# Kernel optimization log

Measured on AMD Instinct MI355X. Metric: run time of the kernel, lower is better.

## Reference

```python
import jax, jax.numpy as jnp
import numpy as np

N, HID, EMB, T_ENC, T_DEC = 10000, 64, 64, 12, 12


def setup_inputs() -> dict:
    key = jax.random.key(0)
    ks = jax.random.split(key, 16)
    s = 0.05  # small init scale (xavier-ish)
    inputs = jax.random.normal(ks[0], (N, T_ENC), dtype=jnp.float32)
    targets = jax.random.normal(ks[1], (N, T_DEC), dtype=jnp.float32)
    a = jax.random.uniform(ks[2], (N, N), dtype=jnp.float32)
    adj_matrix = a / a.sum(axis=1, keepdims=True)  # row-normalized dense learned adjacency
    D_e = EMB + HID  # encoder cell input dim (embedded input + hidden)
    D_d = 1 + HID    # decoder cell input dim (scalar input + hidden)
    return {
        "inputs": inputs,
        "targets": targets,
        "adj_matrix": adj_matrix,
        "W_emb": jax.random.normal(ks[3], (1, EMB)) * s,
        "b_emb": jnp.full((EMB,), 0.1, dtype=jnp.float32),
        "Wg_e": jax.random.normal(ks[4], (3 * D_e, 2 * HID)) * s,
        "bg_e": jnp.zeros((2 * HID,), jnp.float32),
        "Wc_e": jax.random.normal(ks[5], (3 * D_e, HID)) * s,
        "bc_e": jnp.zeros((HID,), jnp.float32),
        "Wg_d": jax.random.normal(ks[6], (3 * D_d, 2 * HID)) * s,
        "bg_d": jnp.zeros((2 * HID,), jnp.float32),
        "Wc_d": jax.random.normal(ks[7], (3 * D_d, HID)) * s,
        "bc_d": jnp.zeros((HID,), jnp.float32),
        "W_pred": jax.random.normal(ks[8], (HID, 1)) * s,
        "b_pred": jnp.full((1,), 0.1, dtype=jnp.float32),
    }


def _gconv(adj, inp, W, b):
    # Chebyshev-style diffusion with max_diffusion_step = 2: [x0, A x0, 2A(A x0) - x0]
    x1 = adj @ inp
    x2 = 2.0 * (adj @ x1) - inp
    return jnp.concatenate([inp, x1, x2], axis=-1) @ W + b


def _dcgru_cell(adj, x, h, Wg, bg, Wc, bc):
    ru = jax.nn.sigmoid(_gconv(adj, jnp.concatenate([x, h], axis=-1), Wg, bg))
    r, u = jnp.split(ru, 2, axis=-1)
    c = jnp.tanh(_gconv(adj, jnp.concatenate([x, r * h], axis=-1), Wc, bc))
    return u * h + (1.0 - u) * c


def reference(inputs, targets, adj_matrix, W_emb, b_emb, Wg_e, bg_e, Wc_e, bc_e,
              Wg_d, bg_d, Wc_d, bc_d, W_pred, b_pred):
    adj = adj_matrix

    def enc_step(h, xt):  # xt: (N,)
        e = xt[:, None] @ W_emb + b_emb  # (N, EMB)
        return _dcgru_cell(adj, e, h, Wg_e, bg_e, Wc_e, bc_e), None

    h0 = jnp.zeros((N, HID), dtype=inputs.dtype)
    h_enc, _ = jax.lax.scan(enc_step, h0, inputs.T)

    def dec_step(carry, _):
        h, x = carry  # x: (N, 1) previous prediction (go symbol = zeros)
        h = _dcgru_cell(adj, x, h, Wg_d, bg_d, Wc_d, bc_d)
        out = h @ W_pred + b_pred  # (N, 1)
        return (h, out), out[:, 0]

    go = jnp.zeros((N, 1), dtype=inputs.dtype)
    _, outs = jax.lax.scan(dec_step, (h_enc, go), None, length=T_DEC)
    return outs.T  # (N, T_DEC)
```

## Files before the change

kernel.cpp:

```cpp
#include <hip/hip_runtime.h>


typedef unsigned short u16;
typedef __attribute__((ext_vector_type(8))) short short8;
typedef __attribute__((ext_vector_type(8))) unsigned short u16x8;
typedef __attribute__((ext_vector_type(4))) unsigned short u16x4;
typedef __attribute__((ext_vector_type(4))) float f32x4;

#define NN 10000
#define P 10112
#define KPAD 10048
#define SPLITS 13
#define KSPLIT 768
#define PLANE 808960

__device__ __forceinline__ u16 f2bf(float f) {
  unsigned u = __float_as_uint(f);
  unsigned r = (u + 0x7FFFu + ((u >> 16) & 1u)) >> 16;
  return (u16)r;
}
__device__ __forceinline__ float bf2f(u16 v) {
  return __uint_as_float((unsigned)v << 16);
}

__device__ __forceinline__ void load_lds16(const void* g, void* l) {
  __builtin_amdgcn_global_load_lds(
      (__attribute__((address_space(1))) void*)(void*)g,
      (__attribute__((address_space(3))) void*)l, 16, 0, 0);
}

__global__ __launch_bounds__(256) void cvt_bf16(const float* __restrict__ a,
                                                u16* __restrict__ o) {
  long i = ((long)blockIdx.x * 256 + threadIdx.x) * 8;
  if (i >= 100000000L) return;
  float4 x = *(const float4*)(a + i);
  float4 y = *(const float4*)(a + i + 4);
  u16x8 v;
  v[0]=f2bf(x.x); v[1]=f2bf(x.y); v[2]=f2bf(x.z); v[3]=f2bf(x.w);
  v[4]=f2bf(y.x); v[5]=f2bf(y.y); v[6]=f2bf(y.z); v[7]=f2bf(y.w);
  *(u16x8*)(o + i) = v;
}

__global__ __launch_bounds__(256) void prep_in(const float* __restrict__ in,
                                               u16* __restrict__ Htin) {
  int m = blockIdx.x * 256 + threadIdx.x;
  int c = blockIdx.y;
  if (m >= NN) return;
  Htin[(size_t)c * P + m] = f2bf(in[(size_t)m * 12 + c]);
}

__global__ void build_w_enc(const float* __restrict__ W, const float* __restrict__ wemb,
    const float* __restrict__ bemb, const float* __restrict__ bsrc, int nout,
    u16* __restrict__ Wt, float* __restrict__ biasout) {
  int j = blockIdx.x, k = threadIdx.x;
  float v = 0.f;
  if (k < 64)        v = W[(64 + k) * nout + j] - W[(320 + k) * nout + j];
  else if (k < 128)  v = W[(192 + (k - 64)) * nout + j];
  else if (k < 192)  v = 2.f * W[(320 + (k - 128)) * nout + j];
  else if (k == 192) { float s = 0; for (int i = 0; i < 64; i++) s += wemb[i] * (W[i*nout+j] - W[(256+i)*nout+j]); v = s; }
  else if (k == 193) { float s = 0; for (int i = 0; i < 64; i++) s += wemb[i] * W[(128+i)*nout+j]; v = s; }
  else if (k == 194) { float s = 0; for (int i = 0; i < 64; i++) s += wemb[i] * W[(256+i)*nout+j]; v = 2.f * s; }
  Wt[j * 256 + k] = f2bf(v);
  if (k == 195) {
    float bb = bsrc[j];
    for (int i = 0; i < 64; i++) bb += bemb[i] * (W[i*nout+j] + W[(128+i)*nout+j] + W[(256+i)*nout+j]);
    biasout[j] = bb;
  }
}

__global__ void build_w_dec(const float* __restrict__ W, int nout, u16* __restrict__ Wt) {
  int j = blockIdx.x, k = threadIdx.x;
  float v = 0.f;
  if (k < 64)        v = W[(1 + k) * nout + j] - W[(131 + k) * nout + j];
  else if (k < 128)  v = W[(66 + (k - 64)) * nout + j];
  else if (k < 192)  v = 2.f * W[(131 + (k - 128)) * nout + j];
  else if (k == 192) v = W[0 * nout + j] - W[130 * nout + j];
  else if (k == 193) v = W[65 * nout + j];
  else if (k == 194) v = 2.f * W[130 * nout + j];
  Wt[j * 256 + k] = f2bf(v);
}

__global__ __launch_bounds__(256) void gemm_bt(
    const u16* __restrict__ A, const u16* __restrict__ Ht,
    u16* __restrict__ PT, int ntiles) {
  __shared__ u16 Al[128 * 64];
  __shared__ u16 Bl[96 * 64];
  int tid = threadIdx.x;
  int wave = tid >> 6, lane = tid & 63, ml = lane & 15, q = lane >> 4;
  int row0 = blockIdx.x * 128;
  int kb = blockIdx.y * KSPLIT;
  int ke = (blockIdx.y == SPLITS - 1) ? KPAD : kb + KSPLIT;
  f32x4 acc[2][5] = {};
  int r8 = tid >> 3, c8 = tid & 7;
  int nrows_b = ntiles * 16;
  int biss = (nrows_b + 31) >> 5;
  for (int k0 = kb; k0 < ke; k0 += 64) {
    int kch = k0 + c8 * 8;
    int kcA = kch > 9992 ? 9992 : kch;
#pragma unroll
    for (int is = 0; is < 4; is++) {
      int row = row0 + is * 32 + r8;
      row = row > 9999 ? 9999 : row;
      load_lds16(A + (size_t)row * NN + kcA, (u16*)Al + is * 2048 + wave * 512);
    }
    for (int is = 0; is < biss; is++) {
      int br = is * 32 + r8;
      br = br >= nrows_b ? nrows_b - 1 : br;
      load_lds16(Ht + (size_t)br * P + k0 + c8 * 8, (u16*)Bl + is * 2048 + wave * 512);
    }
    __syncthreads();
#pragma unroll
    for (int kh = 0; kh < 2; kh++) {
      short8 a0 = *(const short8*)(Al + (wave * 32 + ml) * 64 + kh * 32 + q * 8);
      short8 a1 = *(const short8*)(Al + (wave * 32 + 16 + ml) * 64 + kh * 32 + q * 8);
#pragma unroll
      for (int nt = 0; nt < 5; nt++) {
        if (nt < ntiles) {
          short8 b = *(const short8*)(Bl + (nt * 16 + ml) * 64 + kh * 32 + q * 8);
          acc[0][nt] = __builtin_amdgcn_mfma_f32_16x16x32_bf16(a0, b, acc[0][nt], 0, 0, 0);
          acc[1][nt] = __builtin_amdgcn_mfma_f32_16x16x32_bf16(a1, b, acc[1][nt], 0, 0, 0);
        }
      }
    }
    __syncthreads();
  }
  u16* Pp = PT + (size_t)blockIdx.y * PLANE;
#pragma unroll
  for (int mt = 0; mt < 2; mt++)
#pragma unroll
    for (int nt = 0; nt < 5; nt++)
      if (nt < ntiles) {
        int j = nt * 16 + ml;
        int m = row0 + wave * 32 + mt * 16 + q * 4;
        u16x4 pk;
#pragma unroll
        for (int i = 0; i < 4; i++) pk[i] = f2bf(acc[mt][nt][i]);
        *(u16x4*)(Pp + (size_t)j * P + m) = pk;
      }
}

__global__ __launch_bounds__(256) void red(const u16* __restrict__ PT,
                                           int ncols, u16* __restrict__ T) {
  int nch = ncols * 1264;
  for (int cid = blockIdx.x * 256 + threadIdx.x; cid < nch; cid += gridDim.x * 256) {
    int c = cid / 1264;
    int mb8 = (cid - c * 1264) * 8;
    size_t base = (size_t)c * P + mb8;
    float a[8] = {};
#pragma unroll
    for (int s = 0; s < SPLITS; s++) {
      u16x8 v = *(const u16x8*)(PT + (size_t)s * PLANE + base);
#pragma unroll
      for (int i = 0; i < 8; i++) a[i] += bf2f(v[i]);
    }
    u16x8 o;
#pragma unroll
    for (int i = 0; i < 8; i++) o[i] = (mb8 >= NN) ? (u16)0 : f2bf(a[i]);
    *(u16x8*)(T + base) = o;
  }
}

__global__ __launch_bounds__(256) void cellmm(
    const u16* __restrict__ src0row,
    const u16* __restrict__ T1, const u16* __restrict__ T2,
    const u16* __restrict__ sc0, const u16* __restrict__ sc1,
    const u16* __restrict__ sc2,
    u16* __restrict__ sdec0, u16* __restrict__ sdec1,
    const u16* __restrict__ Wt, const float* __restrict__ bias,
    int ntiles, int mode,
    const float* __restrict__ hx,
    float* __restrict__ ubuf,
    float* __restrict__ hxout,
    u16* __restrict__ rowout,
    u16* __restrict__ htout) {
  __shared__ u16 Al[128 * 64];
  __shared__ u16 Wl[128 * 64];
  int tid = threadIdx.x;
  int wave = tid >> 6, lane = tid & 63, ml = lane & 15, q = lane >> 4;
  int m0 = blockIdx.x * 128;
  f32x4 acc[2][8] = {};
  for (int kc = 0; kc < 4; kc++) {
    if (kc == 0) {
#pragma unroll
      for (int is = 0; is < 4; is++) {
        int row = m0 + is * 32 + (tid >> 3);
        load_lds16(src0row + (size_t)row * 64 + (tid & 7) * 8,
                   (u16*)Al + is * 2048 + wave * 512);
      }
    } else if (kc < 3) {
      const u16* Ts = (kc == 1) ? T1 : T2;
      int c = tid >> 2;
      int mo = (tid & 3) * 32;
      const u16* sp = Ts + (size_t)c * P + m0 + mo;
      u16x8 v0 = *(const u16x8*)(sp);
      u16x8 v1 = *(const u16x8*)(sp + 8);
      u16x8 v2 = *(const u16x8*)(sp + 16);
      u16x8 v3 = *(const u16x8*)(sp + 24);
#pragma unroll
      for (int i = 0; i < 8; i++) {
        Al[(mo + i) * 64 + c]      = v0[i];
        Al[(mo + 8 + i) * 64 + c]  = v1[i];
        Al[(mo + 16 + i) * 64 + c] = v2[i];
        Al[(mo + 24 + i) * 64 + c] = v3[i];
      }
    } else {
      int r = tid >> 1, half = tid & 1;
      int m = m0 + r;
      u16* dst = Al + r * 64 + half * 32;
      if (half == 0) {
        u16 a = sc0[m], b = sc1[m], cc = sc2[m];
        dst[0] = a; dst[1] = b; dst[2] = cc;
#pragma unroll
        for (int jj = 3; jj < 32; jj++) dst[jj] = 0;
        if (sdec0) { sdec0[m] = b; sdec1[m] = cc; }
      } else {
#pragma unroll
        for (int jj = 0; jj < 32; jj++) dst[jj] = 0;
      }
    }
    int wiss = ntiles >> 1;
    for (int is = 0; is < wiss; is++) {
      int jr = is * 32 + (tid >> 3);
      load_lds16(Wt + (size_t)jr * 256 + kc * 64 + (tid & 7) * 8,
                 (u16*)Wl + is * 2048 + wave * 512);
    }
    __syncthreads();
#pragma unroll
    for (int kh = 0; kh < 2; kh++) {
      short8 a0 = *(const short8*)(Al + (wave * 32 + ml) * 64 + kh * 32 + q * 8);
      short8 a1 = *(const short8*)(Al + (wave * 32 + 16 + ml) * 64 + kh * 32 + q * 8);
#pragma unroll
      for (int nt = 0; nt < 8; nt++) {
        if (nt < ntiles) {
          short8 b = *(const short8*)(Wl + (nt * 16 + ml) * 64 + kh * 32 + q * 8);
          acc[0][nt] = __builtin_amdgcn_mfma_f32_16x16x32_bf16(a0, b, acc[0][nt], 0, 0, 0);
          acc[1][nt] = __builtin_amdgcn_mfma_f32_16x16x32_bf16(a1, b, acc[1][nt], 0, 0, 0);
        }
      }
    }
    __syncthreads();
  }
#pragma unroll
  for (int mt = 0; mt < 2; mt++)
#pragma unroll
    for (int nt = 0; nt < 8; nt++)
      if (nt < ntiles) {
        int j = nt * 16 + ml;
        int mb = m0 + wave * 32 + mt * 16 + q * 4;
        u16x4 pk;
        if (mode == 0) {
          if (j < 64) {
#pragma unroll
            for (int i = 0; i < 4; i++) {
              int m = mb + i;
              float g = acc[mt][nt][i] + bias[j];
              float s = 1.f / (1.f + __expf(-g));
              float rv = s * hx[(size_t)m * 64 + j];
              rowout[(size_t)m * 64 + j] = f2bf(rv);
              pk[i] = f2bf(rv);
            }
            if (mb < NN) *(u16x4*)(htout + (size_t)j * P + mb) = pk;
          } else {
#pragma unroll
            for (int i = 0; i < 4; i++) {
              int m = mb + i;
              float g = acc[mt][nt][i] + bias[j];
              ubuf[(size_t)m * 64 + (j - 64)] = 1.f / (1.f + __expf(-g));
            }
          }
        } else {
#pragma unroll
          for (int i = 0; i < 4; i++) {
            int m = mb + i;
            float g = acc[mt][nt][i] + bias[j];
            float cc = 1.f - 2.f / (__expf(2.f * g) + 1.f);
            float uu = ubuf[(size_t)m * 64 + j];
            float hv = hx[(size_t)m * 64 + j];
            float hn = uu * hv + (1.f - uu) * cc;
            hxout[(size_t)m * 64 + j] = hn;
            rowout[(size_t)m * 64 + j] = f2bf(hn);
            pk[i] = f2bf(hn);
          }
          if (mb < NN) *(u16x4*)(htout + (size_t)j * P + mb) = pk;
        }
      }
}

__global__ __launch_bounds__(256) void pred_k(const float* __restrict__ hx,
    const float* __restrict__ Wp, const float* __restrict__ bp,
    float* __restrict__ out, u16* __restrict__ xrow, u16* __restrict__ Ht1,
    int t) {
  int m = blockIdx.x * 256 + threadIdx.x;
  if (m >= P) return;
  const float* h = hx + (size_t)m * 64;
  float s = bp[0];
#pragma unroll
  for (int j = 0; j < 64; j += 4) {
    float4 f = *(const float4*)(h + j);
    s += f.x * Wp[j] + f.y * Wp[j + 1] + f.z * Wp[j + 2] + f.w * Wp[j + 3];
  }
  u16 sb = f2bf(s);
  xrow[m] = sb;
  if (m < NN) {
    Ht1[(size_t)64 * P + m] = sb;
    out[(size_t)m * 12 + t] = s;
  }
}

extern "C" void kernel_launch(void* const* d_in, const int* in_sizes, int n_in,
                              void* d_out, int out_size, void* d_ws, size_t ws_size,
                              hipStream_t stream) {
  const float* inputs = (const float*)d_in[0];
  const float* adj    = (const float*)d_in[2];
  const float* W_emb  = (const float*)d_in[3];
  const float* b_emb  = (const float*)d_in[4];
  const float* Wg_e   = (const float*)d_in[5];
  const float* bg_e   = (const float*)d_in[6];
  const float* Wc_e   = (const float*)d_in[7];
  const float* bc_e   = (const float*)d_in[8];
  const float* Wg_d   = (const float*)d_in[9];
  const float* bg_d   = (const float*)d_in[10];
  const float* Wc_d   = (const float*)d_in[11];
  const float* bc_d   = (const float*)d_in[12];
  const float* W_pred = (const float*)d_in[13];
  const float* b_pred = (const float*)d_in[14];
  float* out = (float*)d_out;
  char* ws = (char*)d_ws;

  size_t off = 0;
  auto alloc = [&](size_t bytes) -> void* {
    void* p = ws + off;
    off += (bytes + 511) & ~(size_t)511;
    return p;
  };
  u16*   A16    = (u16*)  alloc(200000000ULL);
  u16*   PT1    = (u16*)  alloc((size_t)SPLITS * PLANE * 2);
  u16*   PT2    = (u16*)  alloc((size_t)SPLITS * PLANE * 2);
  u16*   Ht1    = (u16*)  alloc((size_t)80 * P * 2);
  u16*   T1     = (u16*)  alloc((size_t)80 * P * 2);
  u16*   T2     = (u16*)  alloc((size_t)80 * P * 2);
  u16*   HtR    = (u16*)  alloc((size_t)64 * P * 2);
  u16*   Htin   = (u16*)  alloc((size_t)16 * P * 2);
  u16*   Ts1    = (u16*)  alloc((size_t)16 * P * 2);
  u16*   Ts2    = (u16*)  alloc((size_t)16 * P * 2);
  float* hx     = (float*)alloc((size_t)P * 64 * 4);
  float* ub     = (float*)alloc((size_t)P * 64 * 4);
  u16*   hxrow  = (u16*)  alloc((size_t)P * 64 * 2);
  u16*   rhrow  = (u16*)  alloc((size_t)P * 64 * 2);
  u16*   xrow   = (u16*)  alloc((size_t)P * 2);
  u16*   sdec   = (u16*)  alloc((size_t)2 * P * 2);
  u16*   Wt_eg  = (u16*)  alloc(128 * 256 * 2);
  u16*   Wt_ec  = (u16*)  alloc(64 * 256 * 2);
  u16*   Wt_dg  = (u16*)  alloc(128 * 256 * 2);
  u16*   Wt_dc  = (u16*)  alloc(64 * 256 * 2);
  float* bias_eg= (float*)alloc(128 * 4);
  float* bias_ec= (float*)alloc(64 * 4);
  if (off > ws_size) return;

  hipMemsetAsync(Ht1, 0, (size_t)80 * P * 2, stream);
  hipMemsetAsync(HtR, 0, (size_t)64 * P * 2, stream);
  hipMemsetAsync(Htin, 0, (size_t)16 * P * 2, stream);
  hipMemsetAsync(hx, 0, (size_t)P * 64 * 4, stream);
  hipMemsetAsync(hxrow, 0, (size_t)P * 64 * 2, stream);
  hipMemsetAsync(xrow, 0, (size_t)P * 2, stream);

  cvt_bf16<<<48829, 256, 0, stream>>>(adj, A16);
  prep_in<<<dim3(40, 12), 256, 0, stream>>>(inputs, Htin);
  build_w_enc<<<128, 256, 0, stream>>>(Wg_e, W_emb, b_emb, bg_e, 128, Wt_eg, bias_eg);
  build_w_enc<<<64, 256, 0, stream>>>(Wc_e, W_emb, b_emb, bc_e, 64, Wt_ec, bias_ec);
  build_w_dec<<<128, 256, 0, stream>>>(Wg_d, 128, Wt_dg);
  build_w_dec<<<64, 256, 0, stream>>>(Wc_d, 64, Wt_dc);

  dim3 ggrid(79, SPLITS);
  gemm_bt<<<ggrid, 256, 0, stream>>>(A16, Htin, PT1, 1);
  red<<<256, 256, 0, stream>>>(PT1, 16, Ts1);
  gemm_bt<<<ggrid, 256, 0, stream>>>(A16, Ts1, PT2, 1);
  red<<<256, 256, 0, stream>>>(PT2, 16, Ts2);

  for (int t = 0; t < 12; t++) {
    gemm_bt<<<ggrid, 256, 0, stream>>>(A16, Ht1, PT1, 4);
    red<<<256, 256, 0, stream>>>(PT1, 64, T1);
    gemm_bt<<<ggrid, 256, 0, stream>>>(A16, T1, PT2, 4);
    red<<<256, 256, 0, stream>>>(PT2, 64, T2);
    cellmm<<<79, 256, 0, stream>>>(hxrow, T1, T2,
        Htin + (size_t)t * P, Ts1 + (size_t)t * P, Ts2 + (size_t)t * P,
        (u16*)nullptr, (u16*)nullptr, Wt_eg, bias_eg, 8, 0,
        hx, ub, (float*)nullptr, rhrow, HtR);
    gemm_bt<<<ggrid, 256, 0, stream>>>(A16, HtR, PT1, 4);
    red<<<256, 256, 0, stream>>>(PT1, 64, T1);
    gemm_bt<<<ggrid, 256, 0, stream>>>(A16, T1, PT2, 4);
    red<<<256, 256, 0, stream>>>(PT2, 64, T2);
    cellmm<<<79, 256, 0, stream>>>(rhrow, T1, T2,
        Htin + (size_t)t * P, Ts1 + (size_t)t * P, Ts2 + (size_t)t * P,
        (u16*)nullptr, (u16*)nullptr, Wt_ec, bias_ec, 4, 1,
        hx, ub, hx, hxrow, Ht1);
  }
  for (int t = 0; t < 12; t++) {
    gemm_bt<<<ggrid, 256, 0, stream>>>(A16, Ht1, PT1, 5);
    red<<<256, 256, 0, stream>>>(PT1, 80, T1);
    gemm_bt<<<ggrid, 256, 0, stream>>>(A16, T1, PT2, 5);
    red<<<256, 256, 0, stream>>>(PT2, 80, T2);
    cellmm<<<79, 256, 0, stream>>>(hxrow, T1, T2,
        xrow, T1 + (size_t)64 * P, T2 + (size_t)64 * P,
        sdec, sdec + P, Wt_dg, bg_d, 8, 0,
        hx, ub, (float*)nullptr, rhrow, HtR);
    gemm_bt<<<ggrid, 256, 0, stream>>>(A16, HtR, PT1, 4);
    red<<<256, 256, 0, stream>>>(PT1, 64, T1);
    gemm_bt<<<ggrid, 256, 0, stream>>>(A16, T1, PT2, 4);
    red<<<256, 256, 0, stream>>>(PT2, 64, T2);
    cellmm<<<79, 256, 0, stream>>>(rhrow, T1, T2,
        xrow, sdec, sdec + P,
        (u16*)nullptr, (u16*)nullptr, Wt_dc, bc_d, 4, 1,
        hx, ub, hx, hxrow, Ht1);
    pred_k<<<40, 256, 0, stream>>>(hx, W_pred, b_pred, out, xrow, Ht1, t);
  }
}
```

Baseline: 6.966 ms.

## Double-buffer and swizzle LDS in adjacency GEMM, template on tile count

Templates the split-K adjacency GEMM on the number of column tiles and double-buffers the A and B LDS tiles. The next K-chunk is prefetched with direct-to-LDS loads while the current one is computed, using hand-tuned vmcnt waits and raw s_barrier instead of __syncthreads. It also XOR-swizzles the LDS layout in both the GEMM and cellmm to avoid bank conflicts on the short8 reads. This is meant to hide global-load latency in the memory-bound adjacency streaming, at the cost of double the LDS use and fragile hand-coded waitcnt counts.

```diff
diff --git a/kernel.cpp b/kernel.cpp
--- a/kernel.cpp
+++ b/kernel.cpp
@@ -80,63 +80,104 @@
   Wt[j * 256 + k] = f2bf(v);
 }
 
-__global__ __launch_bounds__(256) void gemm_bt(
+template <int NT>
+__global__ __launch_bounds__(256) void gemm_bt_t(
     const u16* __restrict__ A, const u16* __restrict__ Ht,
-    u16* __restrict__ PT, int ntiles) {
-  __shared__ u16 Al[128 * 64];
-  __shared__ u16 Bl[96 * 64];
+    u16* __restrict__ PT) {
+  __shared__ u16 Al[2][128 * 64];
+  __shared__ u16 Bl[2][NT * 16 * 64];
   int tid = threadIdx.x;
   int wave = tid >> 6, lane = tid & 63, ml = lane & 15, q = lane >> 4;
   int row0 = blockIdx.x * 128;
   int kb = blockIdx.y * KSPLIT;
   int ke = (blockIdx.y == SPLITS - 1) ? KPAD : kb + KSPLIT;
-  f32x4 acc[2][5] = {};
+  int nch = (ke - kb) >> 6;
+  f32x4 acc[2][NT] = {};
   int r8 = tid >> 3, c8 = tid & 7;
-  int nrows_b = ntiles * 16;
-  int biss = (nrows_b + 31) >> 5;
-  for (int k0 = kb; k0 < ke; k0 += 64) {
-    int kch = k0 + c8 * 8;
-    int kcA = kch > 9992 ? 9992 : kch;
+  int csw = c8 ^ (r8 & 7);
+
+  auto stageA = [&](int buf, int k0) {
+    int kch = k0 + csw * 8;
+    kch = kch > 9992 ? 9992 : kch;
 #pragma unroll
     for (int is = 0; is < 4; is++) {
       int row = row0 + is * 32 + r8;
       row = row > 9999 ? 9999 : row;
-      load_lds16(A + (size_t)row * NN + kcA, (u16*)Al + is * 2048 + wave * 512);
-    }
-    for (int is = 0; is < biss; is++) {
-      int br = is * 32 + r8;
-      br = br >= nrows_b ? nrows_b - 1 : br;
-      load_lds16(Ht + (size_t)br * P + k0 + c8 * 8, (u16*)Bl + is * 2048 + wave * 512);
-    }
-    __syncthreads();
+      load_lds16(A + (size_t)row * NN + kch,
+                 (u16*)&Al[buf][0] + is * 2048 + wave * 512);
+    }
+  };
+  auto stageB = [&](int buf, int k0) {
+    int kk = k0 + csw * 8;
+    if constexpr (NT >= 4) {
+#pragma unroll
+      for (int is = 0; is < 2; is++)
+        load_lds16(Ht + (size_t)(is * 32 + r8) * P + kk,
+                   (u16*)&Bl[buf][0] + is * 2048 + wave * 512);
+    }
+    if constexpr (NT == 5) {
+      if (wave < 2)
+        load_lds16(Ht + (size_t)(64 + r8) * P + kk,
+                   (u16*)&Bl[buf][0] + 4096 + wave * 512);
+    }
+    if constexpr (NT == 1) {
+      if (wave < 2)
+        load_lds16(Ht + (size_t)r8 * P + kk,
+                   (u16*)&Bl[buf][0] + wave * 512);
+    }
+  };
+
+  stageA(0, kb);
+  stageB(0, kb);
+  for (int c = 0; c < nch; c++) {
+    int buf = c & 1;
+    if (c + 1 < nch) {
+      stageA(buf ^ 1, kb + (c + 1) * 64);
+      stageB(buf ^ 1, kb + (c + 1) * 64);
+      __builtin_amdgcn_sched_barrier(0);
+      if constexpr (NT == 5) {
+        if (wave < 2) asm volatile("s_waitcnt vmcnt(7)" ::: "memory");
+        else          asm volatile("s_waitcnt vmcnt(6)" ::: "memory");
+      } else if constexpr (NT == 4) {
+        asm volatile("s_waitcnt vmcnt(6)" ::: "memory");
+      } else {
+        if (wave < 2) asm volatile("s_waitcnt vmcnt(5)" ::: "memory");
+        else          asm volatile("s_waitcnt vmcnt(4)" ::: "memory");
+      }
+    } else {
+      asm volatile("s_waitcnt vmcnt(0)" ::: "memory");
+    }
+    __builtin_amdgcn_sched_barrier(0);
+    __builtin_amdgcn_s_barrier();
+    __builtin_amdgcn_sched_barrier(0);
 #pragma unroll
     for (int kh = 0; kh < 2; kh++) {
-      short8 a0 = *(const short8*)(Al + (wave * 32 + ml) * 64 + kh * 32 + q * 8);
-      short8 a1 = *(const short8*)(Al + (wave * 32 + 16 + ml) * 64 + kh * 32 + q * 8);
-#pragma unroll
-      for (int nt = 0; nt < 5; nt++) {
-        if (nt < ntiles) {
-          short8 b = *(const short8*)(Bl + (nt * 16 + ml) * 64 + kh * 32 + q * 8);
-          acc[0][nt] = __builtin_amdgcn_mfma_f32_16x16x32_bf16(a0, b, acc[0][nt], 0, 0, 0);
-          acc[1][nt] = __builtin_amdgcn_mfma_f32_16x16x32_bf16(a1, b, acc[1][nt], 0, 0, 0);
-        }
-      }
-    }
-    __syncthreads();
+      int s = ((kh * 4 + q) ^ (ml & 7)) * 8;
+      short8 a0 = *(const short8*)(&Al[buf][0] + (wave * 32 + ml) * 64 + s);
+      short8 a1 = *(const short8*)(&Al[buf][0] + (wave * 32 + 16 + ml) * 64 + s);
+#pragma unroll
+      for (int nt = 0; nt < NT; nt++) {
+        short8 b = *(const short8*)(&Bl[buf][0] + (nt * 16 + ml) * 64 + s);
+        acc[0][nt] = __builtin_amdgcn_mfma_f32_16x16x32_bf16(a0, b, acc[0][nt], 0, 0, 0);
+        acc[1][nt] = __builtin_amdgcn_mfma_f32_16x16x32_bf16(a1, b, acc[1][nt], 0, 0, 0);
+      }
+    }
+    __builtin_amdgcn_sched_barrier(0);
+    __builtin_amdgcn_s_barrier();
+    __builtin_amdgcn_sched_barrier(0);
   }
   u16* Pp = PT + (size_t)blockIdx.y * PLANE;
 #pragma unroll
   for (int mt = 0; mt < 2; mt++)
 #pragma unroll
-    for (int nt = 0; nt < 5; nt++)
-      if (nt < ntiles) {
-        int j = nt * 16 + ml;
-        int m = row0 + wave * 32 + mt * 16 + q * 4;
-        u16x4 pk;
-#pragma unroll
-        for (int i = 0; i < 4; i++) pk[i] = f2bf(acc[mt][nt][i]);
-        *(u16x4*)(Pp + (size_t)j * P + m) = pk;
-      }
+    for (int nt = 0; nt < NT; nt++) {
+      int j = nt * 16 + ml;
+      int m = row0 + wave * 32 + mt * 16 + q * 4;
+      u16x4 pk;
+#pragma unroll
+      for (int i = 0; i < 4; i++) pk[i] = f2bf(acc[mt][nt][i]);
+      *(u16x4*)(Pp + (size_t)j * P + m) = pk;
+    }
 }
 
 __global__ __launch_bounds__(256) void red(const u16* __restrict__ PT,
@@ -178,13 +219,15 @@
   int tid = threadIdx.x;
   int wave = tid >> 6, lane = tid & 63, ml = lane & 15, q = lane >> 4;
   int m0 = blockIdx.x * 128;
+  int r8 = tid >> 3, c8 = tid & 7;
+  int csw = c8 ^ (r8 & 7);
   f32x4 acc[2][8] = {};
   for (int kc = 0; kc < 4; kc++) {
     if (kc == 0) {
 #pragma unroll
       for (int is = 0; is < 4; is++) {
-        int row = m0 + is * 32 + (tid >> 3);
-        load_lds16(src0row + (size_t)row * 64 + (tid & 7) * 8,
+        int row = m0 + is * 32 + r8;
+        load_lds16(src0row + (size_t)row * 64 + csw * 8,
                    (u16*)Al + is * 2048 + wave * 512);
       }
     } else if (kc < 3) {
@@ -198,41 +241,44 @@
       u16x8 v3 = *(const u16x8*)(sp + 24);
 #pragma unroll
       for (int i = 0; i < 8; i++) {
-        Al[(mo + i) * 64 + c]      = v0[i];
-        Al[(mo + 8 + i) * 64 + c]  = v1[i];
-        Al[(mo + 16 + i) * 64 + c] = v2[i];
-        Al[(mo + 24 + i) * 64 + c] = v3[i];
+        int cs = c ^ (i << 3);
+        Al[(mo + i) * 64 + cs]      = v0[i];
+        Al[(mo + 8 + i) * 64 + cs]  = v1[i];
+        Al[(mo + 16 + i) * 64 + cs] = v2[i];
+        Al[(mo + 24 + i) * 64 + cs] = v3[i];
       }
     } else {
       int r = tid >> 1, half = tid & 1;
       int m = m0 + r;
-      u16* dst = Al + r * 64 + half * 32;
+      int x = (r & 7) << 3;
+      u16* rowp = Al + r * 64;
       if (half == 0) {
         u16 a = sc0[m], b = sc1[m], cc = sc2[m];
-        dst[0] = a; dst[1] = b; dst[2] = cc;
-#pragma unroll
-        for (int jj = 3; jj < 32; jj++) dst[jj] = 0;
+        rowp[0 ^ x] = a; rowp[1 ^ x] = b; rowp[2 ^ x] = cc;
+#pragma unroll
+        for (int jj = 3; jj < 32; jj++) rowp[jj ^ x] = 0;
         if (sdec0) { sdec0[m] = b; sdec1[m] = cc; }
       } else {
 #pragma unroll
-        for (int jj = 0; jj < 32; jj++) dst[jj] = 0;
+        for (int jj = 32; jj < 64; jj++) rowp[jj ^ x] = 0;
       }
     }
     int wiss = ntiles >> 1;
     for (int is = 0; is < wiss; is++) {
-      int jr = is * 32 + (tid >> 3);
-      load_lds16(Wt + (size_t)jr * 256 + kc * 64 + (tid & 7) * 8,
+      int jr = is * 32 + r8;
+      load_lds16(Wt + (size_t)jr * 256 + kc * 64 + csw * 8,
                  (u16*)Wl + is * 2048 + wave * 512);
     }
     __syncthreads();
 #pragma unroll
     for (int kh = 0; kh < 2; kh++) {
-      short8 a0 = *(const short8*)(Al + (wave * 32 + ml) * 64 + kh * 32 + q * 8);
-      short8 a1 = *(const short8*)(Al + (wave * 32 + 16 + ml) * 64 + kh * 32 + q * 8);
+      int s = ((kh * 4 + q) ^ (ml & 7)) * 8;
+      short8 a0 = *(const short8*)(Al + (wave * 32 + ml) * 64 + s);
+      short8 a1 = *(const short8*)(Al + (wave * 32 + 16 + ml) * 64 + s);
 #pragma unroll
       for (int nt = 0; nt < 8; nt++) {
         if (nt < ntiles) {
-          short8 b = *(const short8*)(Wl + (nt * 16 + ml) * 64 + kh * 32 + q * 8);
+          short8 b = *(const short8*)(Wl + (nt * 16 + ml) * 64 + s);
           acc[0][nt] = __builtin_amdgcn_mfma_f32_16x16x32_bf16(a0, b, acc[0][nt], 0, 0, 0);
           acc[1][nt] = __builtin_amdgcn_mfma_f32_16x16x32_bf16(a1, b, acc[1][nt], 0, 0, 0);
         }
@@ -372,23 +418,23 @@
   build_w_dec<<<64, 256, 0, stream>>>(Wc_d, 64, Wt_dc);
 
   dim3 ggrid(79, SPLITS);
-  gemm_bt<<<ggrid, 256, 0, stream>>>(A16, Htin, PT1, 1);
+  gemm_bt_t<1><<<ggrid, 256, 0, stream>>>(A16, Htin, PT1);
   red<<<256, 256, 0, stream>>>(PT1, 16, Ts1);
-  gemm_bt<<<ggrid, 256, 0, stream>>>(A16, Ts1, PT2, 1);
+  gemm_bt_t<1><<<ggrid, 256, 0, stream>>>(A16, Ts1, PT2);
   red<<<256, 256, 0, stream>>>(PT2, 16, Ts2);
 
   for (int t = 0; t < 12; t++) {
-    gemm_bt<<<ggrid, 256, 0, stream>>>(A16, Ht1, PT1, 4);
+    gemm_bt_t<4><<<ggrid, 256, 0, stream>>>(A16, Ht1, PT1);
     red<<<256, 256, 0, stream>>>(PT1, 64, T1);
-    gemm_bt<<<ggrid, 256, 0, stream>>>(A16, T1, PT2, 4);
+    gemm_bt_t<4><<<ggrid, 256, 0, stream>>>(A16, T1, PT2);
     red<<<256, 256, 0, stream>>>(PT2, 64, T2);
     cellmm<<<79, 256, 0, stream>>>(hxrow, T1, T2,
         Htin + (size_t)t * P, Ts1 + (size_t)t * P, Ts2 + (size_t)t * P,
         (u16*)nullptr, (u16*)nullptr, Wt_eg, bias_eg, 8, 0,
         hx, ub, (float*)nullptr, rhrow, HtR);
-    gemm_bt<<<ggrid, 256, 0, stream>>>(A16, HtR, PT1, 4);
+    gemm_bt_t<4><<<ggrid, 256, 0, stream>>>(A16, HtR, PT1);
     red<<<256, 256, 0, stream>>>(PT1, 64, T1);
-    gemm_bt<<<ggrid, 256, 0, stream>>>(A16, T1, PT2, 4);
+    gemm_bt_t<4><<<ggrid, 256, 0, stream>>>(A16, T1, PT2);
     red<<<256, 256, 0, stream>>>(PT2, 64, T2);
     cellmm<<<79, 256, 0, stream>>>(rhrow, T1, T2,
         Htin + (size_t)t * P, Ts1 + (size_t)t * P, Ts2 + (size_t)t * P,
@@ -396,17 +442,17 @@
         hx, ub, hx, hxrow, Ht1);
   }
   for (int t = 0; t < 12; t++) {
-    gemm_bt<<<ggrid, 256, 0, stream>>>(A16, Ht1, PT1, 5);
+    gemm_bt_t<5><<<ggrid, 256, 0, stream>>>(A16, Ht1, PT1);
     red<<<256, 256, 0, stream>>>(PT1, 80, T1);
-    gemm_bt<<<ggrid, 256, 0, stream>>>(A16, T1, PT2, 5);
+    gemm_bt_t<5><<<ggrid, 256, 0, stream>>>(A16, T1, PT2);
     red<<<256, 256, 0, stream>>>(PT2, 80, T2);
     cellmm<<<79, 256, 0, stream>>>(hxrow, T1, T2,
         xrow, T1 + (size_t)64 * P, T2 + (size_t)64 * P,
         sdec, sdec + P, Wt_dg, bg_d, 8, 0,
         hx, ub, (float*)nullptr, rhrow, HtR);
-    gemm_bt<<<ggrid, 256, 0, stream>>>(A16, HtR, PT1, 4);
+    gemm_bt_t<4><<<ggrid, 256, 0, stream>>>(A16, HtR, PT1);
     red<<<256, 256, 0, stream>>>(PT1, 64, T1);
-    gemm_bt<<<ggrid, 256, 0, stream>>>(A16, T1, PT2, 4);
+    gemm_bt_t<4><<<ggrid, 256, 0, stream>>>(A16, T1, PT2);
     red<<<256, 256, 0, stream>>>(PT2, 64, T2);
     cellmm<<<79, 256, 0, stream>>>(rhrow, T1, T2,
         xrow, sdec, sdec + P,
```

Result: faster. 6.283 ms (-9.8%).
